# Performance work log

Measured on AMD Instinct MI355X. Metric: run time of the kernel, lower is better.

Reference implementation:

```python
import jax, jax.numpy as jnp
import numpy as np
from jax import lax

E, H, D = 1024, 16, 64          # embed_dim, num_heads, head_dim
B, T = 8, 64                    # batch, decode chunk
KV = 4096                       # kv_seq_len -> cache capacity 2*KV
START = 4096                    # start_pos (prefill already filled cache[:START])
THETA = 10000.0


def setup_inputs() -> dict:
    key = jax.random.key(0)
    kx, kck, kcv, kq, kk, kv, ko = jax.random.split(key, 7)
    s = 0.02
    return {
        "x": jax.random.normal(kx, (B, T, E), jnp.float32),
        "cache_keys": jax.random.normal(kck, (B, 2 * KV, H, D), jnp.float32),
        "cache_values": jax.random.normal(kcv, (B, 2 * KV, H, D), jnp.float32),
        "Wq": jax.random.normal(kq, (E, E), jnp.float32) * s,
        "Wk": jax.random.normal(kk, (E, E), jnp.float32) * s,
        "Wv": jax.random.normal(kv, (E, E), jnp.float32) * s,
        "Wo": jax.random.normal(ko, (E, E), jnp.float32) * s,
        "start_pos": START,
    }


def _rope_bug_faithful(x, start_pos):
    # x: (B, T, H, Dd). The source helper unpacks (B,H,T,D)=x.shape on a (B,T,H,D)
    # tensor, so rotation angles are indexed by HEAD index (positions
    # start_pos..start_pos+H-1) and broadcast over the time axis. Reproduced exactly.
    Bn, Tn, Hn, Dd = x.shape
    dh = Dd // 2
    inv_freq = 1.0 / (THETA ** (jnp.arange(dh, dtype=jnp.float32) / dh))
    pos = jnp.arange(Hn, dtype=jnp.float32) + jnp.float32(start_pos)  # (H,)
    ang = pos[:, None] * inv_freq[None, :]                            # (H, dh)
    cos = jnp.cos(ang)[None, None]                                    # (1,1,H,dh)
    sin = jnp.sin(ang)[None, None]
    xr = x.reshape(Bn, Tn, Hn, dh, 2)
    x0, x1 = xr[..., 0], xr[..., 1]
    o0 = x0 * cos - x1 * sin
    o1 = x0 * sin + x1 * cos
    return jnp.stack([o0, o1], axis=-1).reshape(Bn, Tn, Hn, Dd)


def reference(x, cache_keys, cache_values, Wq, Wk, Wv, Wo, start_pos):
    Bn, Tn, C = x.shape
    Hn, Dd = cache_keys.shape[2], cache_keys.shape[3]
    scale = 1.0 / np.sqrt(Dd).astype(np.float32)
    end = start_pos + Tn

    q = (x @ Wq).reshape(Bn, Tn, Hn, Dd)
    k = (x @ Wk).reshape(Bn, Tn, Hn, Dd)
    v = (x @ Wv).reshape(Bn, Tn, Hn, Dd)

    q = _rope_bug_faithful(q, start_pos)
    k = _rope_bug_faithful(k, start_pos)

    # cache append at dynamic offset (detached in source)
    ck = lax.dynamic_update_slice_in_dim(cache_keys, lax.stop_gradient(k), start_pos, axis=1)
    cv = lax.dynamic_update_slice_in_dim(cache_values, lax.stop_gradient(v), start_pos, axis=1)
    k_full = lax.stop_gradient(ck[:, :end])  # (B, S, H, D), S = end
    v_full = lax.stop_gradient(cv[:, :end])

    qh = q.transpose(0, 2, 1, 3)        # (B,H,T,D)
    kh = k_full.transpose(0, 2, 1, 3)   # (B,H,S,D)
    vh = v_full.transpose(0, 2, 1, 3)

    scores = jnp.einsum("bhtd,bhsd->bhts", qh, kh) * scale  # (B,H,T,S)
    i = jnp.arange(Tn)[:, None]
    j = jnp.arange(end)[None, :]
    allowed = j <= (start_pos + i)      # intended causal mask over cache span
    neg = jnp.finfo(scores.dtype).min
    scores = jnp.where(allowed[None, None], scores, neg)
    attn = jax.nn.softmax(scores, axis=-1)
    ctx = jnp.einsum("bhts,bhsd->bhtd", attn, vh)
    out = ctx.transpose(0, 2, 1, 3).reshape(Bn, Tn, C) @ Wo
    return out
```

## Files before the change

kernel.cpp:

```cpp
#include <hip/hip_runtime.h>
#include <hip/hip_bf16.h>
#include <math.h>

typedef __attribute__((ext_vector_type(8))) __bf16 bf16x8;
typedef __attribute__((ext_vector_type(4))) __bf16 bf16x4;
typedef __attribute__((ext_vector_type(4))) float f32x4;

#define EE 1024
#define HH 16
#define DD 64
#define BB 8
#define TT 64
#define NSPLIT 8

__device__ __forceinline__ f32x4 mfma16(bf16x8 a, bf16x8 b, f32x4 c) {
    return __builtin_amdgcn_mfma_f32_16x16x32_bf16(a, b, c, 0, 0, 0);
}

__global__ __launch_bounds__(256) void k_prep(const float* __restrict__ Wq, const float* __restrict__ Wk,
                                              const float* __restrict__ Wv, const float* __restrict__ Wo,
                                              const float* __restrict__ x, const int* __restrict__ sp_ptr,
                                              __bf16* __restrict__ WT, __bf16* __restrict__ xb,
                                              float* __restrict__ cs, float* __restrict__ sn) {
    __shared__ float tile[64][68];
    int bid = blockIdx.x;
    int tid = threadIdx.x;
    if (bid < 1024) {
        int w = bid >> 8, tl = bid & 255;
        int k0 = (tl >> 4) * 64, n0 = (tl & 15) * 64;
        const float* W = (w == 0) ? Wq : (w == 1) ? Wk : (w == 2) ? Wv : Wo;
#pragma unroll
        for (int p = 0; p < 4; ++p) {
            int idx = p * 256 + tid;
            int r = idx >> 4, c4 = (idx & 15) * 4;
            float4 f = *(const float4*)&W[(size_t)(k0 + r) * EE + n0 + c4];
            *(float4*)&tile[r][c4] = f;
        }
        __syncthreads();
        __bf16* out = WT + (size_t)w * EE * EE;
#pragma unroll
        for (int p = 0; p < 2; ++p) {
            int q = p * 256 + tid;
            int r = q >> 3, c8 = (q & 7) * 8;
            bf16x8 v;
#pragma unroll
            for (int j = 0; j < 8; ++j) v[j] = (__bf16)tile[c8 + j][r];
            *(bf16x8*)&out[(size_t)(n0 + r) * EE + k0 + c8] = v;
        }
    } else if (bid < 1280) {
        int i = ((bid - 1024) * 256 + tid) * 8;
        float4 a = *(const float4*)&x[i];
        float4 b = *(const float4*)&x[i + 4];
        bf16x8 v;
        v[0] = (__bf16)a.x; v[1] = (__bf16)a.y; v[2] = (__bf16)a.z; v[3] = (__bf16)a.w;
        v[4] = (__bf16)b.x; v[5] = (__bf16)b.y; v[6] = (__bf16)b.z; v[7] = (__bf16)b.w;
        *(bf16x8*)&xb[i] = v;
    } else {
        int sp = sp_ptr[0];
#pragma unroll
        for (int q = 0; q < 2; ++q) {
            int i = q * 256 + tid;
            int h = i >> 5, p = i & 31;
            double inv = 1.0 / pow(10000.0, (double)p / 32.0);
            double ang = (double)(sp + h) * inv;
            cs[i] = (float)cos(ang);
            sn[i] = (float)sin(ang);
        }
    }
}

__global__ __launch_bounds__(256) void k_qkv(const __bf16* __restrict__ xb, const __bf16* __restrict__ WT,
                                             const float* __restrict__ cs, const float* __restrict__ sn,
                                             __bf16* __restrict__ qws, __bf16* __restrict__ knew,
                                             __bf16* __restrict__ vnew) {
    __shared__ __bf16 a_lds[64][72];
    __shared__ __bf16 b_lds[64][72];
    int bm = blockIdx.x / 48, bn = blockIdx.x % 48;
    int wsel = bn >> 4;
    int n0 = (bn & 15) * 64;
    int m0 = bm * 64;
    const __bf16* Wt = WT + (size_t)wsel * EE * EE;
    int tid = threadIdx.x;
    int wv = tid >> 6, lane = tid & 63;
    int l16 = lane & 15, lhi = lane >> 4;
    int r0 = tid >> 3, c8 = (tid & 7) * 8;

    f32x4 acc[4];
#pragma unroll
    for (int f = 0; f < 4; ++f) acc[f] = (f32x4){0.f, 0.f, 0.f, 0.f};

    bf16x8 ar0 = *(const bf16x8*)&xb[(size_t)(m0 + r0) * EE + c8];
    bf16x8 ar1 = *(const bf16x8*)&xb[(size_t)(m0 + 32 + r0) * EE + c8];
    bf16x8 br0 = *(const bf16x8*)&Wt[(size_t)(n0 + r0) * EE + c8];
    bf16x8 br1 = *(const bf16x8*)&Wt[(size_t)(n0 + 32 + r0) * EE + c8];

    for (int kt = 0; kt < 16; ++kt) {
        __syncthreads();
        *(bf16x8*)&a_lds[r0][c8] = ar0;
        *(bf16x8*)&a_lds[32 + r0][c8] = ar1;
        *(bf16x8*)&b_lds[r0][c8] = br0;
        *(bf16x8*)&b_lds[32 + r0][c8] = br1;
        if (kt < 15) {
            int ko = (kt + 1) * 64;
            ar0 = *(const bf16x8*)&xb[(size_t)(m0 + r0) * EE + ko + c8];
            ar1 = *(const bf16x8*)&xb[(size_t)(m0 + 32 + r0) * EE + ko + c8];
            br0 = *(const bf16x8*)&Wt[(size_t)(n0 + r0) * EE + ko + c8];
            br1 = *(const bf16x8*)&Wt[(size_t)(n0 + 32 + r0) * EE + ko + c8];
        }
        __syncthreads();
        bf16x8 a0 = *(bf16x8*)&a_lds[wv * 16 + l16][lhi * 8];
        bf16x8 a1 = *(bf16x8*)&a_lds[wv * 16 + l16][32 + lhi * 8];
#pragma unroll
        for (int f = 0; f < 4; ++f) {
            bf16x8 b0 = *(bf16x8*)&b_lds[f * 16 + l16][lhi * 8];
            bf16x8 b1 = *(bf16x8*)&b_lds[f * 16 + l16][32 + lhi * 8];
            acc[f] = mfma16(a0, b0, acc[f]);
            acc[f] = mfma16(a1, b1, acc[f]);
        }
    }
    __bf16* dst = (wsel == 0) ? qws : (wsel == 1) ? knew : vnew;
#pragma unroll
    for (int f = 0; f < 4; ++f) {
#pragma unroll
        for (int r = 0; r < 4; ++r) {
            float v = acc[f][r];
            int row = m0 + wv * 16 + lhi * 4 + r;
            int ng = n0 + f * 16 + l16;
            int h = ng >> 6, d = ng & 63;
            float o = v;
            if (wsel < 2) {
                float other = __shfl_xor(v, 1);
                int pp = d >> 1;
                float c = cs[h * 32 + pp], s = sn[h * 32 + pp];
                o = ((d & 1) == 0) ? (v * c - other * s) : (other * s + v * c);
            }
            int b = row >> 6, t = row & 63;
            dst[((size_t)((b * HH + h) * TT + t)) * DD + d] = (__bf16)o;
        }
    }
}

__global__ __launch_bounds__(256, 4) void k_attn(const __bf16* __restrict__ qws, const __bf16* __restrict__ knew,
                                                 const __bf16* __restrict__ vnew,
                                                 const float* __restrict__ ck, const float* __restrict__ cv,
                                                 __bf16* __restrict__ Opart, float2* __restrict__ mlpart) {
    __shared__ __bf16 k_lds[64][72];
    __shared__ __bf16 vT_lds[64][72];
    __shared__ __bf16 p_lds[64][72];
    int bh = blockIdx.x >> 3, split = blockIdx.x & 7;
    int b = bh >> 4, h = bh & 15;
    int tid = threadIdx.x, wv = tid >> 6, lane = tid & 63;
    int l16 = lane & 15, lhi = lane >> 4;
    int rr = tid >> 4, c4 = (tid & 15) * 4;

    bf16x8 qf0, qf1;
    {
        const __bf16* qp = qws + ((size_t)bh * TT + (wv * 16 + l16)) * DD;
        qf0 = *(const bf16x8*)&qp[lhi * 8];
        qf1 = *(const bf16x8*)&qp[32 + lhi * 8];
    }
    f32x4 acc[4];
#pragma unroll
    for (int f = 0; f < 4; ++f) acc[f] = (f32x4){0.f, 0.f, 0.f, 0.f};
    float m[4], l[4];
#pragma unroll
    for (int r = 0; r < 4; ++r) { m[r] = -1e30f; l[r] = 0.f; }

    const float* ckb = ck + (size_t)b * 8192 * EE + h * DD;
    const float* cvb = cv + (size_t)b * 8192 * EE + h * DD;
    int s0 = split * 512;

    auto compute = [&](bool mask) {
        f32x4 sf[4];
#pragma unroll
        for (int f = 0; f < 4; ++f) {
            f32x4 z = (f32x4){0.f, 0.f, 0.f, 0.f};
            bf16x8 b0 = *(bf16x8*)&k_lds[f * 16 + l16][lhi * 8];
            bf16x8 b1 = *(bf16x8*)&k_lds[f * 16 + l16][32 + lhi * 8];
            z = mfma16(qf0, b0, z);
            z = mfma16(qf1, b1, z);
            sf[f] = z;
        }
#pragma unroll
        for (int f = 0; f < 4; ++f) {
#pragma unroll
            for (int r = 0; r < 4; ++r) {
                float sv = sf[f][r] * 0.125f;
                if (mask) {
                    int t_row = wv * 16 + lhi * 4 + r;
                    int s_loc = f * 16 + l16;
                    if (s_loc > t_row) sv = -1e30f;
                }
                sf[f][r] = sv;
            }
        }
        float mt[4];
#pragma unroll
        for (int r = 0; r < 4; ++r)
            mt[r] = fmaxf(fmaxf(sf[0][r], sf[1][r]), fmaxf(sf[2][r], sf[3][r]));
#pragma unroll
        for (int off = 1; off < 16; off <<= 1) {
#pragma unroll
            for (int r = 0; r < 4; ++r) mt[r] = fmaxf(mt[r], __shfl_xor(mt[r], off));
        }
        float fac[4];
#pragma unroll
        for (int r = 0; r < 4; ++r) {
            float mn = fmaxf(m[r], mt[r]);
            fac[r] = __expf(m[r] - mn);
            m[r] = mn;
        }
        float ladd[4] = {0.f, 0.f, 0.f, 0.f};
#pragma unroll
        for (int f = 0; f < 4; ++f) {
#pragma unroll
            for (int r = 0; r < 4; ++r) {
                float pv = __expf(sf[f][r] - m[r]);
                sf[f][r] = pv;
                ladd[r] += pv;
            }
        }
#pragma unroll
        for (int off = 1; off < 16; off <<= 1) {
#pragma unroll
            for (int r = 0; r < 4; ++r) ladd[r] += __shfl_xor(ladd[r], off);
        }
#pragma unroll
        for (int r = 0; r < 4; ++r) l[r] = l[r] * fac[r] + ladd[r];
#pragma unroll
        for (int f = 0; f < 4; ++f)
#pragma unroll
            for (int r = 0; r < 4; ++r) acc[f][r] *= fac[r];
#pragma unroll
        for (int f = 0; f < 4; ++f)
#pragma unroll
            for (int r = 0; r < 4; ++r)
                p_lds[wv * 16 + lhi * 4 + r][f * 16 + l16] = (__bf16)sf[f][r];
        bf16x8 pa0 = *(bf16x8*)&p_lds[wv * 16 + l16][lhi * 8];
        bf16x8 pa1 = *(bf16x8*)&p_lds[wv * 16 + l16][32 + lhi * 8];
#pragma unroll
        for (int f = 0; f < 4; ++f) {
            bf16x8 v0 = *(bf16x8*)&vT_lds[f * 16 + l16][lhi * 8];
            bf16x8 v1 = *(bf16x8*)&vT_lds[f * 16 + l16][32 + lhi * 8];
            acc[f] = mfma16(pa0, v0, acc[f]);
            acc[f] = mfma16(pa1, v1, acc[f]);
        }
    };

    float4 kreg[4], vreg[4];
#pragma unroll
    for (int p = 0; p < 4; ++p) {
        size_t off = (size_t)(s0 + p * 16 + rr) * EE + c4;
        kreg[p] = *(const float4*)&ckb[off];
        vreg[p] = *(const float4*)&cvb[off];
    }

    for (int it = 0; it < 8; ++it) {
#pragma unroll
        for (int p = 0; p < 4; ++p) {
            int r = p * 16 + rr;
            bf16x4 k4 = { (__bf16)kreg[p].x, (__bf16)kreg[p].y, (__bf16)kreg[p].z, (__bf16)kreg[p].w };
            *(bf16x4*)&k_lds[r][c4] = k4;
            vT_lds[c4 + 0][r] = (__bf16)vreg[p].x;
            vT_lds[c4 + 1][r] = (__bf16)vreg[p].y;
            vT_lds[c4 + 2][r] = (__bf16)vreg[p].z;
            vT_lds[c4 + 3][r] = (__bf16)vreg[p].w;
        }
        if (it < 7) {
#pragma unroll
            for (int p = 0; p < 4; ++p) {
                size_t off = (size_t)(s0 + (it + 1) * 64 + p * 16 + rr) * EE + c4;
                kreg[p] = *(const float4*)&ckb[off];
                vreg[p] = *(const float4*)&cvb[off];
            }
        }
        __syncthreads();
        compute(false);
        __syncthreads();
    }

    if (split == 7) {
#pragma unroll
        for (int p = 0; p < 2; ++p) {
            int idx = p * 256 + tid;
            int r = idx >> 3, c8 = (idx & 7) * 8;
            *(bf16x8*)&k_lds[r][c8] = *(const bf16x8*)&knew[((size_t)bh * TT + r) * DD + c8];
            bf16x8 vf = *(const bf16x8*)&vnew[((size_t)bh * TT + r) * DD + c8];
#pragma unroll
            for (int j = 0; j < 8; ++j) vT_lds[c8 + j][r] = vf[j];
        }
        __syncthreads();
        compute(true);
    }

#pragma unroll
    for (int f = 0; f < 4; ++f)
#pragma unroll
        for (int r = 0; r < 4; ++r) {
            int t = wv * 16 + lhi * 4 + r;
            int d = f * 16 + l16;
            Opart[(((size_t)split * 128 + bh) * TT + t) * DD + d] = (__bf16)acc[f][r];
        }
    if (l16 == 0) {
#pragma unroll
        for (int r = 0; r < 4; ++r) {
            int t = wv * 16 + lhi * 4 + r;
            mlpart[((size_t)split * 128 + bh) * TT + t] = make_float2(m[r], l[r]);
        }
    }
}

__global__ __launch_bounds__(256) void k_combine(const __bf16* __restrict__ Opart, const float2* __restrict__ mlpart,
                                                 __bf16* __restrict__ ctxb) {
    int idx = blockIdx.x * 256 + threadIdx.x;
    int d = idx & 63, t = (idx >> 6) & 63, bh = idx >> 12;
    float ms[NSPLIT], ls[NSPLIT];
    float mg = -1e30f;
#pragma unroll
    for (int s = 0; s < NSPLIT; ++s) {
        float2 ml = mlpart[((size_t)s * 128 + bh) * TT + t];
        ms[s] = ml.x; ls[s] = ml.y;
        mg = fmaxf(mg, ms[s]);
    }
    float den = 0.f, num = 0.f;
#pragma unroll
    for (int s = 0; s < NSPLIT; ++s) {
        float w = __expf(ms[s] - mg);
        den += ls[s] * w;
        num += (float)Opart[(((size_t)s * 128 + bh) * TT + t) * DD + d] * w;
    }
    float ctx = num / den;
    int b = bh >> 4, hh = bh & 15;
    ctxb[(size_t)(b * TT + t) * EE + hh * DD + d] = (__bf16)ctx;
}

__global__ __launch_bounds__(256) void k_oproj(const __bf16* __restrict__ ctxb, const __bf16* __restrict__ WoT,
                                               float* __restrict__ out) {
    __shared__ __bf16 a_lds[64][72];
    __shared__ __bf16 b_lds[64][72];
    int bm = blockIdx.x >> 4, bn = blockIdx.x & 15;
    int n0 = bn * 64, m0 = bm * 64;
    int tid = threadIdx.x;
    int wv = tid >> 6, lane = tid & 63;
    int l16 = lane & 15, lhi = lane >> 4;
    int r0 = tid >> 3, c8 = (tid & 7) * 8;
    f32x4 acc[4];
#pragma unroll
    for (int f = 0; f < 4; ++f) acc[f] = (f32x4){0.f, 0.f, 0.f, 0.f};

    bf16x8 ar0 = *(const bf16x8*)&ctxb[(size_t)(m0 + r0) * EE + c8];
    bf16x8 ar1 = *(const bf16x8*)&ctxb[(size_t)(m0 + 32 + r0) * EE + c8];
    bf16x8 br0 = *(const bf16x8*)&WoT[(size_t)(n0 + r0) * EE + c8];
    bf16x8 br1 = *(const bf16x8*)&WoT[(size_t)(n0 + 32 + r0) * EE + c8];

    for (int kt = 0; kt < 16; ++kt) {
        __syncthreads();
        *(bf16x8*)&a_lds[r0][c8] = ar0;
        *(bf16x8*)&a_lds[32 + r0][c8] = ar1;
        *(bf16x8*)&b_lds[r0][c8] = br0;
        *(bf16x8*)&b_lds[32 + r0][c8] = br1;
        if (kt < 15) {
            int ko = (kt + 1) * 64;
            ar0 = *(const bf16x8*)&ctxb[(size_t)(m0 + r0) * EE + ko + c8];
            ar1 = *(const bf16x8*)&ctxb[(size_t)(m0 + 32 + r0) * EE + ko + c8];
            br0 = *(const bf16x8*)&WoT[(size_t)(n0 + r0) * EE + ko + c8];
            br1 = *(const bf16x8*)&WoT[(size_t)(n0 + 32 + r0) * EE + ko + c8];
        }
        __syncthreads();
        bf16x8 a0 = *(bf16x8*)&a_lds[wv * 16 + l16][lhi * 8];
        bf16x8 a1 = *(bf16x8*)&a_lds[wv * 16 + l16][32 + lhi * 8];
#pragma unroll
        for (int f = 0; f < 4; ++f) {
            bf16x8 b0 = *(bf16x8*)&b_lds[f * 16 + l16][lhi * 8];
            bf16x8 b1 = *(bf16x8*)&b_lds[f * 16 + l16][32 + lhi * 8];
            acc[f] = mfma16(a0, b0, acc[f]);
            acc[f] = mfma16(a1, b1, acc[f]);
        }
    }
#pragma unroll
    for (int f = 0; f < 4; ++f)
#pragma unroll
        for (int r = 0; r < 4; ++r) {
            int row = m0 + wv * 16 + lhi * 4 + r;
            out[(size_t)row * EE + n0 + f * 16 + l16] = acc[f][r];
        }
}

extern "C" void kernel_launch(void* const* d_in, const int* in_sizes, int n_in,
                              void* d_out, int out_size, void* d_ws, size_t ws_size,
                              hipStream_t stream) {
    const float* x  = (const float*)d_in[0];
    const float* ck = (const float*)d_in[1];
    const float* cv = (const float*)d_in[2];
    const float* Wq = (const float*)d_in[3];
    const float* Wk = (const float*)d_in[4];
    const float* Wv = (const float*)d_in[5];
    const float* Wo = (const float*)d_in[6];
    const int* sp   = (const int*)d_in[7];
    float* out = (float*)d_out;

    char* p = (char*)d_ws;
    float* cs = (float*)p;              p += 2048;
    float* sn = (float*)p;              p += 2048;
    __bf16* xb = (__bf16*)p;            p += (size_t)512 * 1024 * 2;
    __bf16* WT = (__bf16*)p;            p += (size_t)4 * 1024 * 1024 * 2;
    __bf16* qws = (__bf16*)p;           p += (size_t)524288 * 2;
    __bf16* knew = (__bf16*)p;          p += (size_t)524288 * 2;
    __bf16* vnew = (__bf16*)p;          p += (size_t)524288 * 2;
    __bf16* Opart = (__bf16*)p;         p += (size_t)NSPLIT * 128 * 64 * 64 * 2;
    float2* mlpart = (float2*)p;        p += (size_t)NSPLIT * 8192 * 8;
    __bf16* ctxb = (__bf16*)p;          p += (size_t)524288 * 2;

    k_prep<<<1281, 256, 0, stream>>>(Wq, Wk, Wv, Wo, x, sp, WT, xb, cs, sn);
    k_qkv<<<384, 256, 0, stream>>>(xb, WT, cs, sn, qws, knew, vnew);
    k_attn<<<BB * HH * NSPLIT, 256, 0, stream>>>(qws, knew, vnew, ck, cv, Opart, mlpart);
    k_combine<<<2048, 256, 0, stream>>>(Opart, mlpart, ctxb);
    k_oproj<<<128, 256, 0, stream>>>(ctxb, WT + (size_t)3 * 1024 * 1024, out);
}
```

Before: 91.92 us.

## Remap GEMM blocks per XCD and vectorize V transpose stores into LDS

The QKV and output-projection GEMMs now map block indices so that blocks landing on the same XCD share the same weight column tiles, which should improve L2 reuse of the weights. In the attention kernel, each thread now loads four consecutive V rows, so it can pack a 4-element transposed bf16 vector and write it to LDS in one store instead of four scalar stores. The V LDS row pitch is changed from 72 to 68 to suit the new store pattern. The trade-offs are a possible change in LDS bank conflicts on the MFMA reads and a global load pattern for V that now spans more rows per wave.

```diff
diff --git a/kernel.cpp b/kernel.cpp
--- a/kernel.cpp
+++ b/kernel.cpp
@@ -75,7 +75,9 @@
                                              __bf16* __restrict__ vnew) {
     __shared__ __bf16 a_lds[64][72];
     __shared__ __bf16 b_lds[64][72];
-    int bm = blockIdx.x / 48, bn = blockIdx.x % 48;
+    int xcd = blockIdx.x & 7, idx = blockIdx.x >> 3;
+    int bn = xcd * 6 + idx % 6;
+    int bm = idx / 6;
     int wsel = bn >> 4;
     int n0 = (bn & 15) * 64;
     int m0 = bm * 64;
@@ -145,13 +147,13 @@
                                                  const float* __restrict__ ck, const float* __restrict__ cv,
                                                  __bf16* __restrict__ Opart, float2* __restrict__ mlpart) {
     __shared__ __bf16 k_lds[64][72];
-    __shared__ __bf16 vT_lds[64][72];
+    __shared__ __bf16 vT_lds[64][68];
     __shared__ __bf16 p_lds[64][72];
     int bh = blockIdx.x >> 3, split = blockIdx.x & 7;
     int b = bh >> 4, h = bh & 15;
     int tid = threadIdx.x, wv = tid >> 6, lane = tid & 63;
     int l16 = lane & 15, lhi = lane >> 4;
-    int rr = tid >> 4, c4 = (tid & 15) * 4;
+    int g = tid >> 4, m4 = (tid & 15) * 4;
 
     bf16x8 qf0, qf1;
     {
@@ -247,32 +249,33 @@
         }
     };
 
-    float4 kreg[4], vreg[4];
-#pragma unroll
-    for (int p = 0; p < 4; ++p) {
-        size_t off = (size_t)(s0 + p * 16 + rr) * EE + c4;
-        kreg[p] = *(const float4*)&ckb[off];
-        vreg[p] = *(const float4*)&cvb[off];
-    }
+    f32x4 kreg[4], vreg[4];
+#pragma unroll
+    for (int p = 0; p < 4; ++p)
+        kreg[p] = *(const f32x4*)&ckb[(size_t)(s0 + p * 16 + g) * EE + m4];
+#pragma unroll
+    for (int i = 0; i < 4; ++i)
+        vreg[i] = *(const f32x4*)&cvb[(size_t)(s0 + 4 * g + i) * EE + m4];
 
     for (int it = 0; it < 8; ++it) {
 #pragma unroll
         for (int p = 0; p < 4; ++p) {
-            int r = p * 16 + rr;
-            bf16x4 k4 = { (__bf16)kreg[p].x, (__bf16)kreg[p].y, (__bf16)kreg[p].z, (__bf16)kreg[p].w };
-            *(bf16x4*)&k_lds[r][c4] = k4;
-            vT_lds[c4 + 0][r] = (__bf16)vreg[p].x;
-            vT_lds[c4 + 1][r] = (__bf16)vreg[p].y;
-            vT_lds[c4 + 2][r] = (__bf16)vreg[p].z;
-            vT_lds[c4 + 3][r] = (__bf16)vreg[p].w;
+            bf16x4 k4 = { (__bf16)kreg[p][0], (__bf16)kreg[p][1], (__bf16)kreg[p][2], (__bf16)kreg[p][3] };
+            *(bf16x4*)&k_lds[p * 16 + g][m4] = k4;
+        }
+#pragma unroll
+        for (int j = 0; j < 4; ++j) {
+            bf16x4 tv = { (__bf16)vreg[0][j], (__bf16)vreg[1][j], (__bf16)vreg[2][j], (__bf16)vreg[3][j] };
+            *(bf16x4*)&vT_lds[m4 + j][4 * g] = tv;
         }
         if (it < 7) {
-#pragma unroll
-            for (int p = 0; p < 4; ++p) {
-                size_t off = (size_t)(s0 + (it + 1) * 64 + p * 16 + rr) * EE + c4;
-                kreg[p] = *(const float4*)&ckb[off];
-                vreg[p] = *(const float4*)&cvb[off];
-            }
+            int sb = s0 + (it + 1) * 64;
+#pragma unroll
+            for (int p = 0; p < 4; ++p)
+                kreg[p] = *(const f32x4*)&ckb[(size_t)(sb + p * 16 + g) * EE + m4];
+#pragma unroll
+            for (int i = 0; i < 4; ++i)
+                vreg[i] = *(const f32x4*)&cvb[(size_t)(sb + 4 * g + i) * EE + m4];
         }
         __syncthreads();
         compute(false);
@@ -338,7 +341,9 @@
                                                float* __restrict__ out) {
     __shared__ __bf16 a_lds[64][72];
     __shared__ __bf16 b_lds[64][72];
-    int bm = blockIdx.x >> 4, bn = blockIdx.x & 15;
+    int xcd = blockIdx.x & 7, idx = blockIdx.x >> 3;
+    int bn = xcd * 2 + (idx & 1);
+    int bm = idx >> 1;
     int n0 = bn * 64, m0 = bm * 64;
     int tid = threadIdx.x;
     int wv = tid >> 6, lane = tid & 63;
```

New measurement: 87.35 us. -5.0%, faster.
